# Kernel optimization log

Measured on AMD Instinct MI355X. Metric: run time of the kernel, lower is better.

## Reference

```python
import jax, jax.numpy as jnp
import numpy as np

N_NODES = 50000


def _gcn_norm(edge_index, num_nodes):
    """PyG GCNConv normalization: add self-loops, symmetric deg^{-1/2} weights."""
    loops = jnp.arange(num_nodes, dtype=edge_index.dtype)
    src = jnp.concatenate([edge_index[0], loops])
    dst = jnp.concatenate([edge_index[1], loops])
    deg = jax.ops.segment_sum(jnp.ones_like(dst, dtype=jnp.float32), dst,
                              num_segments=num_nodes)
    dinv = jax.lax.rsqrt(jnp.maximum(deg, 1.0))  # self-loops guarantee deg>=1
    norm = dinv[src] * dinv[dst]                 # [E + N]
    return src, dst, norm


def _gcn_conv(x, W, b, src, dst, norm, num_nodes):
    h = x @ W                                    # [N, out] dense GEMM
    msg = h[src] * norm[:, None]                 # gather + scale
    agg = jax.ops.segment_sum(msg, dst, num_segments=num_nodes)
    return agg + b


def setup_inputs() -> dict:
    key = jax.random.key(0)
    ks = jax.random.split(key, 8)
    d = 128
    scale = 1.0 / np.sqrt(d)
    emb = jax.random.normal(ks[0], (N_NODES, d), dtype=jnp.float32)
    W1 = jax.random.normal(ks[1], (d, d), dtype=jnp.float32) * scale
    W2 = jax.random.normal(ks[2], (d, d), dtype=jnp.float32) * scale
    W3 = jax.random.normal(ks[3], (d, d), dtype=jnp.float32) * scale
    b1 = jnp.zeros((d,), dtype=jnp.float32)
    b2 = jnp.zeros((d,), dtype=jnp.float32)
    b3 = jnp.zeros((d,), dtype=jnp.float32)
    edge_index = jax.random.randint(ks[4], (2, 600000), 0, N_NODES, dtype=jnp.int64)
    return {"emb": emb, "W1": W1, "b1": b1, "W2": W2, "b2": b2,
            "W3": W3, "b3": b3, "edge_index": edge_index}


def reference(emb, W1, b1, W2, b2, W3, b3, edge_index):
    # Eval-mode forward: F.dropout(training=False) is identity.
    src, dst, norm = _gcn_norm(edge_index, N_NODES)
    x = emb
    x = jax.nn.relu(_gcn_conv(x, W1, b1, src, dst, norm, N_NODES))
    x = jax.nn.relu(_gcn_conv(x, W2, b2, src, dst, norm, N_NODES))
    x = _gcn_conv(x, W3, b3, src, dst, norm, N_NODES)
    x = x.at[0].set(0.0)  # x[0] = zeros(x.shape[1])
    return x
```

## Files before the change

### kernel.cpp

```cpp
#include <hip/hip_runtime.h>
#include <hip/hip_fp16.h>

#define NN 50000
#define D 128
#define STRIDE 64

typedef __attribute__((ext_vector_type(16))) float f32x16;
typedef _Float16 h16;
typedef __attribute__((ext_vector_type(8))) _Float16 h16x8;

struct alignas(16) H8 { h16 h[8]; };

typedef const __attribute__((address_space(1))) void gvoid;
typedef __attribute__((address_space(3))) void lvoid;

__global__ __launch_bounds__(256) void wprep_kernel(const float* __restrict__ W1,
                                                    const float* __restrict__ W2,
                                                    const float* __restrict__ W3,
                                                    h16* __restrict__ Wsp,
                                                    int* __restrict__ cnt) {
    if (blockIdx.x < 3) {
        const float* W = blockIdx.x == 0 ? W1 : (blockIdx.x == 1 ? W2 : W3);
        h16* dst = Wsp + blockIdx.x * 32768;
        const int l  = threadIdx.x & 63;
        const int ct = threadIdx.x >> 6;
        const int n  = ct * 32 + (l & 31);
        const int lh = l >> 5;
#pragma unroll
        for (int ks = 0; ks < 8; ks++) {
            const int kbase = ks * 16 + lh * 8;
            H8 hi8, lo8;
#pragma unroll
            for (int j = 0; j < 8; j++) {
                float w = W[(kbase + j) * D + n];
                h16 hi = (h16)w;
                hi8.h[j] = hi;
                lo8.h[j] = (h16)(w - (float)hi);
            }
            const int base = ((ks * 4 + ct) * 64 + l) * 8;
            *(H8*)(dst + base)         = hi8;
            *(H8*)(dst + base + 16384) = lo8;
        }
    }
    for (int i = blockIdx.x * 256 + threadIdx.x; i < NN; i += 56 * 256) cnt[i] = 0;
}

__global__ __launch_bounds__(256) void fill_kernel(const int* __restrict__ srcA,
                                                   const int* __restrict__ dstA,
                                                   int* __restrict__ cnt,
                                                   int* __restrict__ slots, int nquad) {
    int t = blockIdx.x * 256 + threadIdx.x;
    if (t >= nquad) return;
    int4 s4 = ((const int4*)srcA)[t];
    int4 d4 = ((const int4*)dstA)[t];
    int p0 = atomicAdd(&cnt[d4.x], 1);
    int p1 = atomicAdd(&cnt[d4.y], 1);
    int p2 = atomicAdd(&cnt[d4.z], 1);
    int p3 = atomicAdd(&cnt[d4.w], 1);
    if (p0 < STRIDE - 4) slots[d4.x * STRIDE + p0] = s4.x;
    if (p1 < STRIDE - 4) slots[d4.y * STRIDE + p1] = s4.y;
    if (p2 < STRIDE - 4) slots[d4.z * STRIDE + p2] = s4.z;
    if (p3 < STRIDE - 4) slots[d4.w * STRIDE + p3] = s4.w;
}

__global__ __launch_bounds__(256, 2) void gemm_mfma(const void* __restrict__ Xv, int x_is_f32,
                                                    const h16* __restrict__ Wsp,
                                                    h16* __restrict__ H, int M) {
    __shared__ h16 Ws[32768];
    {
        const int t = threadIdx.x;
#pragma unroll
        for (int i = 0; i < 16; i++) {
            const int off = (i * 256 + t) * 8;
            __builtin_amdgcn_global_load_lds((gvoid*)(Wsp + off), (lvoid*)(Ws + off),
                                             16, 0, 0);
        }
    }
    __syncthreads();

    const int wave = threadIdx.x >> 6;
    const int lane = threadIdx.x & 63;
    const int row0 = blockIdx.x * 128 + wave * 32;
    const int arow = min(row0 + (lane & 31), M - 1);
    const int koff = (lane >> 5) * 8;

    f32x16 acc[4] = {};

#pragma unroll
    for (int ks = 0; ks < 8; ks++) {
        h16x8 ahi, alo;
        if (x_is_f32) {
            const float* p = (const float*)Xv + (size_t)arow * D + koff + ks * 16;
            float4 fa = *(const float4*)p;
            float4 fb = *(const float4*)(p + 4);
            float f[8] = {fa.x, fa.y, fa.z, fa.w, fb.x, fb.y, fb.z, fb.w};
#pragma unroll
            for (int j = 0; j < 8; j++) {
                h16 hi = (h16)f[j];
                ahi[j] = hi;
                alo[j] = (h16)(f[j] - (float)hi);
            }
        } else {
            const h16* p = (const h16*)Xv + (size_t)arow * D + koff + ks * 16;
            ahi = *(const h16x8*)p;
        }
#pragma unroll
        for (int ct = 0; ct < 4; ct++) {
            const int base = ((ks * 4 + ct) * 64 + lane) * 8;
            h16x8 bhi = *(const h16x8*)(Ws + base);
            h16x8 blo = *(const h16x8*)(Ws + base + 16384);
            acc[ct] = __builtin_amdgcn_mfma_f32_32x32x16_f16(ahi, bhi, acc[ct], 0, 0, 0);
            acc[ct] = __builtin_amdgcn_mfma_f32_32x32x16_f16(ahi, blo, acc[ct], 0, 0, 0);
            if (x_is_f32)
                acc[ct] = __builtin_amdgcn_mfma_f32_32x32x16_f16(alo, bhi, acc[ct], 0, 0, 0);
        }
    }

    const int col0 = lane & 31;
    const int rbase = row0 + 4 * (lane >> 5);
#pragma unroll
    for (int ct = 0; ct < 4; ct++) {
#pragma unroll
        for (int r = 0; r < 16; r++) {
            int row = rbase + (r & 3) + 8 * (r >> 2);
            if (row < M) H[(size_t)row * D + ct * 32 + col0] = (h16)acc[ct][r];
        }
    }
}

__global__ __launch_bounds__(256) void agg_kernel(const h16* __restrict__ H,
                                                  const int* __restrict__ cnt,
                                                  const int* __restrict__ slots,
                                                  const float* __restrict__ bias,
                                                  h16* __restrict__ out16,
                                                  float* __restrict__ out32,
                                                  int mode) {
    const int lane = threadIdx.x & 63;
    const int node = blockIdx.x * 4 + (threadIdx.x >> 6);
    const int q    = lane >> 4;
    const int col  = (lane & 15) * 8;

    const int c = __builtin_amdgcn_readfirstlane(cnt[node]);
    const float di = rsqrtf((float)c + 1.0f);
    const int sbase = node * STRIDE;
    const int pc = min((c + 8) & ~7, STRIDE);

    float aA[8] = {0.f, 0.f, 0.f, 0.f, 0.f, 0.f, 0.f, 0.f};
    float aB[8] = {0.f, 0.f, 0.f, 0.f, 0.f, 0.f, 0.f, 0.f};

    for (int p = 0; p < pc; p += 8) {
        const int ja = p + q;
        const int jb = p + 4 + q;
        int sa = slots[sbase + ja];
        int sb = slots[sbase + jb];
        sa = (ja < c) ? sa : node;
        sb = (jb < c) ? sb : node;
        float wa = (ja < c) ? rsqrtf((float)cnt[sa] + 1.0f) : ((ja == c) ? di : 0.f);
        float wb = (jb < c) ? rsqrtf((float)cnt[sb] + 1.0f) : ((jb == c) ? di : 0.f);
        h16x8 va = *(const h16x8*)(H + (size_t)sa * D + col);
        h16x8 vb = *(const h16x8*)(H + (size_t)sb * D + col);
#pragma unroll
        for (int j = 0; j < 8; j++) {
            aA[j] = fmaf(wa, (float)va[j], aA[j]);
            aB[j] = fmaf(wb, (float)vb[j], aB[j]);
        }
    }

#pragma unroll
    for (int j = 0; j < 8; j++) {
        float v = aA[j] + aB[j];
        v += __shfl_xor(v, 16, 64);
        v += __shfl_xor(v, 32, 64);
        aA[j] = v;
    }

    if (lane < 16) {
        float4 bb0 = *(const float4*)(bias + col);
        float4 bb1 = *(const float4*)(bias + col + 4);
        float r[8];
        r[0] = fmaf(di, aA[0], bb0.x); r[1] = fmaf(di, aA[1], bb0.y);
        r[2] = fmaf(di, aA[2], bb0.z); r[3] = fmaf(di, aA[3], bb0.w);
        r[4] = fmaf(di, aA[4], bb1.x); r[5] = fmaf(di, aA[5], bb1.y);
        r[6] = fmaf(di, aA[6], bb1.z); r[7] = fmaf(di, aA[7], bb1.w);
        if (mode == 0) {
            h16x8 o;
#pragma unroll
            for (int j = 0; j < 8; j++) o[j] = (h16)fmaxf(r[j], 0.f);
            *(h16x8*)(out16 + (size_t)node * D + col) = o;
        } else {
            if (node == 0) {
#pragma unroll
                for (int j = 0; j < 8; j++) r[j] = 0.f;
            }
            *(float4*)(out32 + (size_t)node * D + col)     = make_float4(r[0], r[1], r[2], r[3]);
            *(float4*)(out32 + (size_t)node * D + col + 4) = make_float4(r[4], r[5], r[6], r[7]);
        }
    }
}


extern "C" void kernel_launch(void* const* d_in, const int* in_sizes, int n_in,
                              void* d_out, int out_size, void* d_ws, size_t ws_size,
                              hipStream_t stream) {
    const float* emb = (const float*)d_in[0];
    const float* W1  = (const float*)d_in[1];
    const float* b1  = (const float*)d_in[2];
    const float* W2  = (const float*)d_in[3];
    const float* b2  = (const float*)d_in[4];
    const float* W3  = (const float*)d_in[5];
    const float* b3  = (const float*)d_in[6];
    const int*   ei  = (const int*)d_in[7];

    const int E = in_sizes[7] / 2;
    const int* srcA = ei;
    const int* dstA = ei + E;
    float* out = (float*)d_out;

    char* ws = (char*)d_ws;
    size_t off = 0;
    auto alloc = [&](size_t bytes) -> void* {
        void* p = ws + off;
        off = (off + bytes + 255) & ~(size_t)255;
        return p;
    };
    h16* h      = (h16*)alloc((size_t)NN * D * 2);
    h16* x16    = (h16*)alloc((size_t)NN * D * 2);
    int* cnt    = (int*)alloc((size_t)NN * 4);
    int* slots  = (int*)alloc((size_t)NN * STRIDE * 4);
    h16* Wsp    = (h16*)alloc((size_t)3 * 32768 * 2);

    const int T = 256;
    const int gemm_grid = (NN + 127) / 128;
    const int agg_grid  = NN / 4;
    const int nquad = E / 4;

    wprep_kernel<<<56, T, 0, stream>>>(W1, W2, W3, Wsp, cnt);
    gemm_mfma<<<gemm_grid, T, 0, stream>>>(emb, 1, Wsp, h, NN);
    fill_kernel<<<(nquad + T - 1) / T, T, 0, stream>>>(srcA, dstA, cnt, slots, nquad);
    agg_kernel<<<agg_grid, T, 0, stream>>>(h, cnt, slots, b1, x16, nullptr, 0);
    gemm_mfma<<<gemm_grid, T, 0, stream>>>(x16, 0, Wsp + 32768, h, NN);
    agg_kernel<<<agg_grid, T, 0, stream>>>(h, cnt, slots, b2, x16, nullptr, 0);
    gemm_mfma<<<gemm_grid, T, 0, stream>>>(x16, 0, Wsp + 65536, h, NN);
    agg_kernel<<<agg_grid, T, 0, stream>>>(h, cnt, slots, b3, nullptr, out, 1);
}
```

Before: 257.7 us.

## Stage GEMM output via LDS, prefetch slot indices, widen fill and split weight prep

The GEMM epilogue now writes accumulators into shared memory and then emits coalesced 16-byte row stores instead of scattered 2-byte stores. The aggregation loop software-prefetches the next pair of neighbor slot indices to hide index-load latency. The fill kernel handles eight edges per thread, and weight prep is split across 24 blocks, one per k-slice of each matrix, instead of three serial blocks. These target global-store efficiency, latency in the gather loop and prep-kernel serialization. The cost is an extra barrier and LDS reuse in the GEMM, plus more registers per thread in fill.

```diff
diff --git a/kernel.cpp b/kernel.cpp
--- a/kernel.cpp
+++ b/kernel.cpp
@@ -19,48 +19,56 @@
                                                     const float* __restrict__ W3,
                                                     h16* __restrict__ Wsp,
                                                     int* __restrict__ cnt) {
-    if (blockIdx.x < 3) {
-        const float* W = blockIdx.x == 0 ? W1 : (blockIdx.x == 1 ? W2 : W3);
-        h16* dst = Wsp + blockIdx.x * 32768;
-        const int l  = threadIdx.x & 63;
-        const int ct = threadIdx.x >> 6;
-        const int n  = ct * 32 + (l & 31);
-        const int lh = l >> 5;
-#pragma unroll
-        for (int ks = 0; ks < 8; ks++) {
-            const int kbase = ks * 16 + lh * 8;
-            H8 hi8, lo8;
-#pragma unroll
-            for (int j = 0; j < 8; j++) {
-                float w = W[(kbase + j) * D + n];
-                h16 hi = (h16)w;
-                hi8.h[j] = hi;
-                lo8.h[j] = (h16)(w - (float)hi);
-            }
-            const int base = ((ks * 4 + ct) * 64 + l) * 8;
-            *(H8*)(dst + base)         = hi8;
-            *(H8*)(dst + base + 16384) = lo8;
-        }
-    }
-    for (int i = blockIdx.x * 256 + threadIdx.x; i < NN; i += 56 * 256) cnt[i] = 0;
+    const int b  = blockIdx.x;
+    const int w  = b >> 3;
+    const int ks = b & 7;
+    const float* W = w == 0 ? W1 : (w == 1 ? W2 : W3);
+    h16* dst = Wsp + w * 32768;
+    const int l  = threadIdx.x & 63;
+    const int ct = threadIdx.x >> 6;
+    const int n  = ct * 32 + (l & 31);
+    const int lh = l >> 5;
+    const int kbase = ks * 16 + lh * 8;
+    H8 hi8, lo8;
+#pragma unroll
+    for (int j = 0; j < 8; j++) {
+        float wv = W[(kbase + j) * D + n];
+        h16 hi = (h16)wv;
+        hi8.h[j] = hi;
+        lo8.h[j] = (h16)(wv - (float)hi);
+    }
+    const int base = ((ks * 4 + ct) * 64 + l) * 8;
+    *(H8*)(dst + base)         = hi8;
+    *(H8*)(dst + base + 16384) = lo8;
+    for (int i = b * 256 + threadIdx.x; i < NN; i += 24 * 256) cnt[i] = 0;
 }
 
 __global__ __launch_bounds__(256) void fill_kernel(const int* __restrict__ srcA,
                                                    const int* __restrict__ dstA,
                                                    int* __restrict__ cnt,
-                                                   int* __restrict__ slots, int nquad) {
+                                                   int* __restrict__ slots, int noct) {
     int t = blockIdx.x * 256 + threadIdx.x;
-    if (t >= nquad) return;
-    int4 s4 = ((const int4*)srcA)[t];
-    int4 d4 = ((const int4*)dstA)[t];
-    int p0 = atomicAdd(&cnt[d4.x], 1);
-    int p1 = atomicAdd(&cnt[d4.y], 1);
-    int p2 = atomicAdd(&cnt[d4.z], 1);
-    int p3 = atomicAdd(&cnt[d4.w], 1);
-    if (p0 < STRIDE - 4) slots[d4.x * STRIDE + p0] = s4.x;
-    if (p1 < STRIDE - 4) slots[d4.y * STRIDE + p1] = s4.y;
-    if (p2 < STRIDE - 4) slots[d4.z * STRIDE + p2] = s4.z;
-    if (p3 < STRIDE - 4) slots[d4.w * STRIDE + p3] = s4.w;
+    if (t >= noct) return;
+    int4 sa = ((const int4*)srcA)[2 * t];
+    int4 sb = ((const int4*)srcA)[2 * t + 1];
+    int4 da = ((const int4*)dstA)[2 * t];
+    int4 db = ((const int4*)dstA)[2 * t + 1];
+    int p0 = atomicAdd(&cnt[da.x], 1);
+    int p1 = atomicAdd(&cnt[da.y], 1);
+    int p2 = atomicAdd(&cnt[da.z], 1);
+    int p3 = atomicAdd(&cnt[da.w], 1);
+    int p4 = atomicAdd(&cnt[db.x], 1);
+    int p5 = atomicAdd(&cnt[db.y], 1);
+    int p6 = atomicAdd(&cnt[db.z], 1);
+    int p7 = atomicAdd(&cnt[db.w], 1);
+    if (p0 < STRIDE - 4) slots[da.x * STRIDE + p0] = sa.x;
+    if (p1 < STRIDE - 4) slots[da.y * STRIDE + p1] = sa.y;
+    if (p2 < STRIDE - 4) slots[da.z * STRIDE + p2] = sa.z;
+    if (p3 < STRIDE - 4) slots[da.w * STRIDE + p3] = sa.w;
+    if (p4 < STRIDE - 4) slots[db.x * STRIDE + p4] = sb.x;
+    if (p5 < STRIDE - 4) slots[db.y * STRIDE + p5] = sb.y;
+    if (p6 < STRIDE - 4) slots[db.z * STRIDE + p6] = sb.z;
+    if (p7 < STRIDE - 4) slots[db.w * STRIDE + p7] = sb.w;
 }
 
 __global__ __launch_bounds__(256, 2) void gemm_mfma(const void* __restrict__ Xv, int x_is_f32,
@@ -116,14 +124,27 @@
         }
     }
 
-    const int col0 = lane & 31;
-    const int rbase = row0 + 4 * (lane >> 5);
-#pragma unroll
-    for (int ct = 0; ct < 4; ct++) {
-#pragma unroll
-        for (int r = 0; r < 16; r++) {
-            int row = rbase + (r & 3) + 8 * (r >> 2);
-            if (row < M) H[(size_t)row * D + ct * 32 + col0] = (h16)acc[ct][r];
+    __syncthreads();
+    {
+        h16* C_lds = Ws;
+        const int col0 = lane & 31;
+        const int lr0  = 4 * (lane >> 5);
+#pragma unroll
+        for (int ct = 0; ct < 4; ct++) {
+#pragma unroll
+            for (int r = 0; r < 16; r++) {
+                const int lrow = lr0 + (r & 3) + 8 * (r >> 2);
+                C_lds[(wave * 32 + lrow) * D + ct * 32 + col0] = (h16)acc[ct][r];
+            }
+        }
+        const h16* src = C_lds + wave * 32 * D;
+        h16* gdst = H + (size_t)row0 * D;
+#pragma unroll
+        for (int j = 0; j < 8; j++) {
+            const int i = j * 64 + lane;
+            const int row = row0 + (i >> 4);
+            if (row < M)
+                *(h16x8*)(gdst + (size_t)i * 8) = *(const h16x8*)(src + i * 8);
         }
     }
 }
@@ -148,22 +169,26 @@
     float aA[8] = {0.f, 0.f, 0.f, 0.f, 0.f, 0.f, 0.f, 0.f};
     float aB[8] = {0.f, 0.f, 0.f, 0.f, 0.f, 0.f, 0.f, 0.f};
 
+    int sa = slots[sbase + q];
+    int sb = slots[sbase + 4 + q];
+
     for (int p = 0; p < pc; p += 8) {
+        int sa_n = slots[sbase + min(p + 8 + q, STRIDE - 1)];
+        int sb_n = slots[sbase + min(p + 12 + q, STRIDE - 1)];
         const int ja = p + q;
         const int jb = p + 4 + q;
-        int sa = slots[sbase + ja];
-        int sb = slots[sbase + jb];
-        sa = (ja < c) ? sa : node;
-        sb = (jb < c) ? sb : node;
-        float wa = (ja < c) ? rsqrtf((float)cnt[sa] + 1.0f) : ((ja == c) ? di : 0.f);
-        float wb = (jb < c) ? rsqrtf((float)cnt[sb] + 1.0f) : ((jb == c) ? di : 0.f);
-        h16x8 va = *(const h16x8*)(H + (size_t)sa * D + col);
-        h16x8 vb = *(const h16x8*)(H + (size_t)sb * D + col);
+        const int ca = (ja < c) ? sa : node;
+        const int cb = (jb < c) ? sb : node;
+        float wa = (ja < c) ? rsqrtf((float)cnt[ca] + 1.0f) : ((ja == c) ? di : 0.f);
+        float wb = (jb < c) ? rsqrtf((float)cnt[cb] + 1.0f) : ((jb == c) ? di : 0.f);
+        h16x8 va = *(const h16x8*)(H + (size_t)ca * D + col);
+        h16x8 vb = *(const h16x8*)(H + (size_t)cb * D + col);
 #pragma unroll
         for (int j = 0; j < 8; j++) {
             aA[j] = fmaf(wa, (float)va[j], aA[j]);
             aB[j] = fmaf(wb, (float)vb[j], aB[j]);
         }
+        sa = sa_n; sb = sb_n;
     }
 
 #pragma unroll
@@ -232,11 +257,11 @@
     const int T = 256;
     const int gemm_grid = (NN + 127) / 128;
     const int agg_grid  = NN / 4;
-    const int nquad = E / 4;
-
-    wprep_kernel<<<56, T, 0, stream>>>(W1, W2, W3, Wsp, cnt);
+    const int noct = E / 8;
+
+    wprep_kernel<<<24, T, 0, stream>>>(W1, W2, W3, Wsp, cnt);
     gemm_mfma<<<gemm_grid, T, 0, stream>>>(emb, 1, Wsp, h, NN);
-    fill_kernel<<<(nquad + T - 1) / T, T, 0, stream>>>(srcA, dstA, cnt, slots, nquad);
+    fill_kernel<<<(noct + T - 1) / T, T, 0, stream>>>(srcA, dstA, cnt, slots, noct);
     agg_kernel<<<agg_grid, T, 0, stream>>>(h, cnt, slots, b1, x16, nullptr, 0);
     gemm_mfma<<<gemm_grid, T, 0, stream>>>(x16, 0, Wsp + 32768, h, NN);
     agg_kernel<<<agg_grid, T, 0, stream>>>(h, cnt, slots, b2, x16, nullptr, 0);
```

New measurement: 252.1 us. 2.2% less time.
